# Kernel optimization log

Measured on AMD Instinct MI355X. Metric: run time of the kernel, lower is better.

## Reference

```python
import jax, jax.numpy as jnp
import numpy as np

NEG_SLOPE = 0.2


def gat_layer(x, src, dst, W, a_src, a_dst, b):
    # x: [N, Fin]; W: [Fin, H*C]; a_src/a_dst: [H, C]; b: [H*C]
    N = x.shape[0]
    H, C = a_src.shape
    h = (x @ W).reshape(N, H, C)                      # [N,H,C]
    s = jnp.einsum('nhc,hc->nh', h, a_src)            # alpha_src per node
    d = jnp.einsum('nhc,hc->nh', h, a_dst)            # alpha_dst per node
    e = jax.nn.leaky_relu(s[src] + d[dst], NEG_SLOPE) # [E,H]
    # segment softmax over incoming edges of each dst node
    m = jax.ops.segment_max(e, dst, num_segments=N)   # [N,H]
    ex = jnp.exp(e - m[dst])
    denom = jax.ops.segment_sum(ex, dst, num_segments=N)
    alpha = ex / (denom[dst] + 1e-16)                 # [E,H]
    out = jax.ops.segment_sum(h[src] * alpha[:, :, None], dst, num_segments=N)
    return out.reshape(N, H * C) + b                  # concat heads (H=1)


def setup_inputs() -> dict:
    key = jax.random.key(0)
    ks = jax.random.split(key, 16)
    N, E, Fin, Hid, Out, Hd = 100000, 1600000, 128, 64, 64, 1
    inp = {
        'x': jax.random.normal(ks[0], (N, Fin), dtype=jnp.float32),
        'edge_index': jax.random.randint(ks[1], (2, E), 0, N, dtype=jnp.int64),
    }
    def glorot(k, shape):
        fan = shape[0] + shape[-1]
        return jax.random.normal(k, shape, dtype=jnp.float32) * np.sqrt(2.0 / fan)
    inp['W1'] = glorot(ks[2], (Fin, Hd * Hid))
    inp['a1_src'] = glorot(ks[3], (Hd, Hid))
    inp['a1_dst'] = glorot(ks[4], (Hd, Hid))
    inp['b1'] = jnp.zeros((Hd * Hid,), dtype=jnp.float32)
    inp['W2'] = glorot(ks[5], (Hid, Hd * Hid))
    inp['a2_src'] = glorot(ks[6], (Hd, Hid))
    inp['a2_dst'] = glorot(ks[7], (Hd, Hid))
    inp['b2'] = jnp.zeros((Hd * Hid,), dtype=jnp.float32)
    inp['W3'] = glorot(ks[8], (Hid, Hd * Hid))
    inp['a3_src'] = glorot(ks[9], (Hd, Hid))
    inp['a3_dst'] = glorot(ks[10], (Hd, Hid))
    inp['b3'] = jnp.zeros((Hd * Hid,), dtype=jnp.float32)
    inp['fc_w'] = glorot(ks[11], (Hid, Out))
    inp['fc_b'] = jnp.zeros((Out,), dtype=jnp.float32)
    return inp


def reference(x, edge_index, W1, a1_src, a1_dst, b1, W2, a2_src, a2_dst, b2,
              W3, a3_src, a3_dst, b3, fc_w, fc_b):
    N = x.shape[0]
    loop = jnp.arange(N, dtype=edge_index.dtype)      # PyG add_self_loops
    src = jnp.concatenate([edge_index[0], loop])
    dst = jnp.concatenate([edge_index[1], loop])
    h = gat_layer(x, src, dst, W1, a1_src, a1_dst, b1)
    h = gat_layer(h, src, dst, W2, a2_src, a2_dst, b2)
    h = gat_layer(h, src, dst, W3, a3_src, a3_dst, b3)
    return h @ fc_w + fc_b
```

## Files before the change

### kernel.cpp

```cpp
#include <hip/hip_runtime.h>
#include <hip/hip_bf16.h>

typedef unsigned short u16;
typedef unsigned int u32;

__device__ __forceinline__ float wred_max(float v) {
    #pragma unroll
    for (int m = 32; m; m >>= 1) v = fmaxf(v, __shfl_xor(v, m, 64));
    return v;
}
__device__ __forceinline__ float wred_sum(float v) {
    #pragma unroll
    for (int m = 32; m; m >>= 1) v += __shfl_xor(v, m, 64);
    return v;
}
__device__ __forceinline__ u16 f2b(float f) {
    u32 u = __float_as_uint(f);
    u32 r = (u + 0x7FFFu + ((u >> 16) & 1u)) >> 16;
    return (u16)r;
}
__device__ __forceinline__ float blo(u32 u) { return __uint_as_float(u << 16); }
__device__ __forceinline__ float bhi(u32 u) { return __uint_as_float(u & 0xFFFF0000u); }

#define BIN_SHIFT 8
#define BIN_CHUNK 4096
#define MAXBINS 512

__global__ __launch_bounds__(256) void k_bin_gemm1(
    const int* __restrict__ ei, int E, int nbins, int binb, int cap,
    int* __restrict__ gcount, unsigned* __restrict__ rec,
    const float* __restrict__ in, const float* __restrict__ W,
    const float* __restrict__ asrc, const float* __restrict__ adst,
    u16* __restrict__ outh, float* __restrict__ sv, float* __restrict__ dv, int N)
{
    constexpr int K = 128;
    __shared__ float smem[64 * 64 + 64 * 64];
    const int tid = threadIdx.x;

    if (blockIdx.x < (unsigned)binb) {
        int* hist = (int*)smem;
        int* base = hist + MAXBINS;
        const int cbase = blockIdx.x * BIN_CHUNK;
        const int EN = E + N;

        for (int b = tid; b < nbins; b += 256) hist[b] = 0;
        __syncthreads();

        int srcs[16], dsts[16];
        #pragma unroll
        for (int i = 0; i < 16; i++) {
            int t = cbase + i * 256 + tid;
            int s = 0, d = -1;
            if (t < EN) {
                if (t < E) { s = ei[t]; d = ei[E + t]; }
                else       { s = t - E; d = s; }
                atomicAdd(&hist[d >> BIN_SHIFT], 1);
            }
            srcs[i] = s; dsts[i] = d;
        }
        __syncthreads();
        for (int b = tid; b < nbins; b += 256) {
            int h = hist[b];
            base[b] = h ? atomicAdd(&gcount[b], h) : 0;
        }
        __syncthreads();
        for (int b = tid; b < nbins; b += 256) hist[b] = 0;
        __syncthreads();
        #pragma unroll
        for (int i = 0; i < 16; i++) {
            int d = dsts[i];
            if (d >= 0) {
                int bin = d >> BIN_SHIFT;
                int r = atomicAdd(&hist[bin], 1);
                int idx = bin * cap + base[bin] + r;
                rec[idx] = (unsigned)srcs[i] | ((unsigned)(d & ((1 << BIN_SHIFT) - 1)) << 24);
            }
        }
        return;
    }

    float* Wl = smem;
    float* Xl = smem + 64 * 64;
    const int base = (blockIdx.x - binb) * 64;

    const int c4 = (tid & 15) << 2;
    const int r4 = (tid >> 4) << 2;

    float acc[4][4];
    #pragma unroll
    for (int i = 0; i < 4; i++)
        #pragma unroll
        for (int j = 0; j < 4; j++) acc[i][j] = 0.f;

    #define FMA4(i, XC, WV) \
        acc[i][0] += (XC) * (WV).x; acc[i][1] += (XC) * (WV).y; \
        acc[i][2] += (XC) * (WV).z; acc[i][3] += (XC) * (WV).w;

    for (int kt = 0; kt < K; kt += 64) {
        __syncthreads();
        for (int i = tid * 4; i < 64 * 64; i += 1024)
            *reinterpret_cast<float4*>(Wl + i) =
                *reinterpret_cast<const float4*>(W + (size_t)kt * 64 + i);
        for (int i = tid * 4; i < 64 * 64; i += 1024) {
            int node = i >> 6;
            int k = i & 63;
            float4 v = make_float4(0.f, 0.f, 0.f, 0.f);
            int gn = base + node;
            if (gn < N) v = *reinterpret_cast<const float4*>(in + (size_t)gn * K + kt + k);
            *reinterpret_cast<float4*>(Xl + node * 64 + (k ^ ((node & 7) << 2))) = v;
        }
        __syncthreads();

        for (int k0 = 0; k0 < 64; k0 += 4) {
            float4 wv0 = *reinterpret_cast<const float4*>(Wl + (k0 + 0) * 64 + c4);
            float4 wv1 = *reinterpret_cast<const float4*>(Wl + (k0 + 1) * 64 + c4);
            float4 wv2 = *reinterpret_cast<const float4*>(Wl + (k0 + 2) * 64 + c4);
            float4 wv3 = *reinterpret_cast<const float4*>(Wl + (k0 + 3) * 64 + c4);
            #pragma unroll
            for (int i = 0; i < 4; i++) {
                int node = r4 + i;
                float4 xv = *reinterpret_cast<const float4*>(
                    Xl + node * 64 + (k0 ^ ((node & 7) << 2)));
                FMA4(i, xv.x, wv0)
                FMA4(i, xv.y, wv1)
                FMA4(i, xv.z, wv2)
                FMA4(i, xv.w, wv3)
            }
        }
    }
    #undef FMA4

    const float4 as = *reinterpret_cast<const float4*>(asrc + c4);
    const float4 ad = *reinterpret_cast<const float4*>(adst + c4);
    #pragma unroll
    for (int i = 0; i < 4; i++) {
        int node = base + r4 + i;
        float ps = acc[i][0] * as.x + acc[i][1] * as.y
                 + acc[i][2] * as.z + acc[i][3] * as.w;
        float pd = acc[i][0] * ad.x + acc[i][1] * ad.y
                 + acc[i][2] * ad.z + acc[i][3] * ad.w;
        #pragma unroll
        for (int m = 1; m < 16; m <<= 1) {
            ps += __shfl_xor(ps, m, 64);
            pd += __shfl_xor(pd, m, 64);
        }
        if (node < N) {
            ushort4 o;
            o.x = f2b(acc[i][0]); o.y = f2b(acc[i][1]);
            o.z = f2b(acc[i][2]); o.w = f2b(acc[i][3]);
            *reinterpret_cast<ushort4*>(outh + ((size_t)node << 6) + c4) = o;
            if ((tid & 15) == 0) { sv[node] = ps; dv[node] = pd; }
        }
    }
}

__global__ __launch_bounds__(256) void k_unbin(
    const unsigned* __restrict__ rec, const int* __restrict__ gcount,
    int cap, int N, int* __restrict__ deg, int* __restrict__ colvp)
{
    __shared__ int cnt[1 << BIN_SHIFT];
    const int b = blockIdx.x;
    const int tid = threadIdx.x;
    const int node0 = b << BIN_SHIFT;
    cnt[tid] = 0;
    __syncthreads();
    int count = min(gcount[b], cap);
    for (int i = tid; i < count; i += 256) {
        unsigned r = rec[(size_t)b * cap + i];
        int s  = (int)(r & 0xFFFFFFu);
        int dl = (int)(r >> 24);
        int pos = atomicAdd(&cnt[dl], 1);
        if (pos < 64) colvp[((size_t)(node0 + dl) << 6) + pos] = s;
    }
    __syncthreads();
    int n = node0 + tid;
    if (n < N) deg[n] = min(cnt[tid], 64);
}

template<bool FUSE_SD>
__global__ __launch_bounds__(256) void k_gemm64(
    const float* __restrict__ in, const float* __restrict__ W,
    const float* __restrict__ asrc, const float* __restrict__ adst,
    const float* __restrict__ bias, void* __restrict__ out_,
    float* __restrict__ sv, float* __restrict__ dv, int N)
{
    constexpr int K = 64;
    __shared__ float Wl[K * 64];
    __shared__ float Xl[64 * K];
    const int tid  = threadIdx.x;
    const int base = blockIdx.x * 64;

    for (int i = tid * 4; i < K * 64; i += 1024)
        *reinterpret_cast<float4*>(Wl + i) = *reinterpret_cast<const float4*>(W + i);

    for (int i = tid * 4; i < 64 * K; i += 1024) {
        int node = i >> 6;
        int k = i & (K - 1);
        float4 v = make_float4(0.f, 0.f, 0.f, 0.f);
        int gn = base + node;
        if (gn < N) v = *reinterpret_cast<const float4*>(in + (size_t)gn * K + k);
        *reinterpret_cast<float4*>(Xl + node * K + (k ^ ((node & 7) << 2))) = v;
    }
    __syncthreads();

    const int c4 = (tid & 15) << 2;
    const int r4 = (tid >> 4) << 2;

    float acc[4][4];
    #pragma unroll
    for (int i = 0; i < 4; i++)
        #pragma unroll
        for (int j = 0; j < 4; j++) acc[i][j] = 0.f;

    #define FMA4(i, XC, WV) \
        acc[i][0] += (XC) * (WV).x; acc[i][1] += (XC) * (WV).y; \
        acc[i][2] += (XC) * (WV).z; acc[i][3] += (XC) * (WV).w;

    for (int k0 = 0; k0 < K; k0 += 4) {
        float4 wv0 = *reinterpret_cast<const float4*>(Wl + (k0 + 0) * 64 + c4);
        float4 wv1 = *reinterpret_cast<const float4*>(Wl + (k0 + 1) * 64 + c4);
        float4 wv2 = *reinterpret_cast<const float4*>(Wl + (k0 + 2) * 64 + c4);
        float4 wv3 = *reinterpret_cast<const float4*>(Wl + (k0 + 3) * 64 + c4);
        #pragma unroll
        for (int i = 0; i < 4; i++) {
            int node = r4 + i;
            float4 xv = *reinterpret_cast<const float4*>(
                Xl + node * K + (k0 ^ ((node & 7) << 2)));
            FMA4(i, xv.x, wv0)
            FMA4(i, xv.y, wv1)
            FMA4(i, xv.z, wv2)
            FMA4(i, xv.w, wv3)
        }
    }
    #undef FMA4

    if (FUSE_SD) {
        u16* outh = (u16*)out_;
        const float4 as = *reinterpret_cast<const float4*>(asrc + c4);
        const float4 ad = *reinterpret_cast<const float4*>(adst + c4);
        #pragma unroll
        for (int i = 0; i < 4; i++) {
            int node = base + r4 + i;
            float ps = acc[i][0] * as.x + acc[i][1] * as.y
                     + acc[i][2] * as.z + acc[i][3] * as.w;
            float pd = acc[i][0] * ad.x + acc[i][1] * ad.y
                     + acc[i][2] * ad.z + acc[i][3] * ad.w;
            #pragma unroll
            for (int m = 1; m < 16; m <<= 1) {
                ps += __shfl_xor(ps, m, 64);
                pd += __shfl_xor(pd, m, 64);
            }
            if (node < N) {
                ushort4 o;
                o.x = f2b(acc[i][0]); o.y = f2b(acc[i][1]);
                o.z = f2b(acc[i][2]); o.w = f2b(acc[i][3]);
                *reinterpret_cast<ushort4*>(outh + ((size_t)node << 6) + c4) = o;
                if ((tid & 15) == 0) { sv[node] = ps; dv[node] = pd; }
            }
        }
    } else {
        float* outf = (float*)out_;
        const float4 bv = *reinterpret_cast<const float4*>(bias + c4);
        #pragma unroll
        for (int i = 0; i < 4; i++) {
            int node = base + r4 + i;
            if (node < N) {
                *reinterpret_cast<float4*>(outf + ((size_t)node << 6) + c4) =
                    make_float4(acc[i][0] + bv.x, acc[i][1] + bv.y,
                                acc[i][2] + bv.z, acc[i][3] + bv.w);
            }
        }
    }
}

__global__ __launch_bounds__(256) void k_agg(
    const int* __restrict__ colv, const int* __restrict__ degarr,
    const float* __restrict__ sv, const float* __restrict__ dv,
    const u16* __restrict__ hb, const float* __restrict__ bias,
    float* __restrict__ out, int N)
{
    int n = blockIdx.x * 4 + (threadIdx.x >> 6);
    if (n >= N) return;
    int lane = threadIdx.x & 63;
    int r0 = n << 6;
    int deg = min(degarr[n], 64);
    float dn = dv[n];

    int sj = 0; float e = -3.4e38f;
    if (lane < deg) {
        sj = colv[r0 + lane];
        float t = sv[sj] + dn;
        e = t > 0.f ? t : 0.2f * t;
    }
    float m = wred_max(e);
    float p = (lane < deg) ? __expf(e - m) : 0.f;
    float den = wred_sum(p) + 1e-16f;
    p *= (1.0f / den);

    const int g  = lane >> 3;
    const int c8 = (lane & 7) << 3;
    const u16* hbase = hb + c8;
    const int dm1 = deg - 1;

    float acc[8];
    #pragma unroll
    for (int i = 0; i < 8; i++) acc[i] = 0.f;

    for (int j0 = 0; j0 < deg; j0 += 32) {
        int m0 = j0 + g;
        int m1 = m0 + 8, m2 = m0 + 16, m3 = m0 + 24;
        int cc0 = min(m0, dm1), cc1 = min(m1, dm1);
        int cc2 = min(m2, dm1), cc3 = min(m3, dm1);
        float a0 = __shfl(p, cc0, 64); int s0 = __shfl(sj, cc0, 64);
        float a1 = __shfl(p, cc1, 64); int s1 = __shfl(sj, cc1, 64);
        float a2 = __shfl(p, cc2, 64); int s2 = __shfl(sj, cc2, 64);
        float a3 = __shfl(p, cc3, 64); int s3 = __shfl(sj, cc3, 64);
        if (m1 > dm1) a1 = 0.f;
        if (m2 > dm1) a2 = 0.f;
        if (m3 > dm1) a3 = 0.f;
        uint4 u0 = make_uint4(0u,0u,0u,0u), u1 = u0, u2 = u0, u3 = u0;
        if (m0 <= dm1) u0 = *reinterpret_cast<const uint4*>(hbase + ((size_t)s0 << 6));
        if (m1 <= dm1) u1 = *reinterpret_cast<const uint4*>(hbase + ((size_t)s1 << 6));
        if (m2 <= dm1) u2 = *reinterpret_cast<const uint4*>(hbase + ((size_t)s2 << 6));
        if (m3 <= dm1) u3 = *reinterpret_cast<const uint4*>(hbase + ((size_t)s3 << 6));
        acc[0] += a0 * blo(u0.x); acc[1] += a0 * bhi(u0.x);
        acc[2] += a0 * blo(u0.y); acc[3] += a0 * bhi(u0.y);
        acc[4] += a0 * blo(u0.z); acc[5] += a0 * bhi(u0.z);
        acc[6] += a0 * blo(u0.w); acc[7] += a0 * bhi(u0.w);
        acc[0] += a1 * blo(u1.x); acc[1] += a1 * bhi(u1.x);
        acc[2] += a1 * blo(u1.y); acc[3] += a1 * bhi(u1.y);
        acc[4] += a1 * blo(u1.z); acc[5] += a1 * bhi(u1.z);
        acc[6] += a1 * blo(u1.w); acc[7] += a1 * bhi(u1.w);
        acc[0] += a2 * blo(u2.x); acc[1] += a2 * bhi(u2.x);
        acc[2] += a2 * blo(u2.y); acc[3] += a2 * bhi(u2.y);
        acc[4] += a2 * blo(u2.z); acc[5] += a2 * bhi(u2.z);
        acc[6] += a2 * blo(u2.w); acc[7] += a2 * bhi(u2.w);
        acc[0] += a3 * blo(u3.x); acc[1] += a3 * bhi(u3.x);
        acc[2] += a3 * blo(u3.y); acc[3] += a3 * bhi(u3.y);
        acc[4] += a3 * blo(u3.z); acc[5] += a3 * bhi(u3.z);
        acc[6] += a3 * blo(u3.w); acc[7] += a3 * bhi(u3.w);
    }
    #pragma unroll
    for (int mm = 8; mm <= 32; mm <<= 1) {
        #pragma unroll
        for (int i = 0; i < 8; i++) acc[i] += __shfl_xor(acc[i], mm, 64);
    }
    if (lane < 8) {
        const float4 b0 = *reinterpret_cast<const float4*>(bias + c8);
        const float4 b1 = *reinterpret_cast<const float4*>(bias + c8 + 4);
        *reinterpret_cast<float4*>(out + ((size_t)n << 6) + c8) =
            make_float4(acc[0] + b0.x, acc[1] + b0.y, acc[2] + b0.z, acc[3] + b0.w);
        *reinterpret_cast<float4*>(out + ((size_t)n << 6) + c8 + 4) =
            make_float4(acc[4] + b1.x, acc[5] + b1.y, acc[6] + b1.z, acc[7] + b1.w);
    }
}

extern "C" void kernel_launch(void* const* d_in, const int* in_sizes, int n_in,
                              void* d_out, int out_size, void* d_ws, size_t ws_size,
                              hipStream_t stream)
{
    const float* x   = (const float*)d_in[0];
    const int*   ei  = (const int*)d_in[1];
    const float* W1  = (const float*)d_in[2];
    const float* a1s = (const float*)d_in[3];
    const float* a1d = (const float*)d_in[4];
    const float* b1  = (const float*)d_in[5];
    const float* W2  = (const float*)d_in[6];
    const float* a2s = (const float*)d_in[7];
    const float* a2d = (const float*)d_in[8];
    const float* b2  = (const float*)d_in[9];
    const float* W3  = (const float*)d_in[10];
    const float* a3s = (const float*)d_in[11];
    const float* a3d = (const float*)d_in[12];
    const float* b3  = (const float*)d_in[13];
    const float* fw  = (const float*)d_in[14];
    const float* fb  = (const float*)d_in[15];

    const int Hid = in_sizes[3];
    const int Fin = in_sizes[2] / Hid;
    const int N   = in_sizes[0] / Fin;
    const int E   = in_sizes[1] / 2;
    const int EN  = E + N;
    (void)n_in; (void)out_size; (void)ws_size;

    char* p = (char*)d_ws;
    auto alloc = [&](size_t bytes) -> char* {
        char* r = p; p += (bytes + 255) & ~(size_t)255; return r;
    };
    float* sv = (float*)alloc((size_t)N * 4);
    float* dv = (float*)alloc((size_t)N * 4);
    u16*   h0 = (u16*)  alloc((size_t)N * 64 * 2);
    float* h1 = (float*)alloc((size_t)N * 64 * 4);
    int*   deg = (int*)  alloc((size_t)N * 4);
    int*   gcount = (int*)alloc((size_t)MAXBINS * 4);
    int*   colvp  = (int*)alloc((size_t)N * 64 * 4);

    const int nbins = (N + (1 << BIN_SHIFT) - 1) >> BIN_SHIFT;
    const int binb  = (EN + BIN_CHUNK - 1) / BIN_CHUNK;
    int cap = ((EN / nbins) * 2 + 127) & ~127;
    unsigned* rec = (unsigned*)h1;

    int gb = (N + 63) / 64;
    int ab = (N + 3) / 4;
    float* out = (float*)d_out;

    hipMemsetAsync(gcount, 0, (size_t)nbins * 4, stream);
    k_bin_gemm1<<<binb + gb, 256, 0, stream>>>(ei, E, nbins, binb, cap, gcount, rec,
                                               x, W1, a1s, a1d, h0, sv, dv, N);
    k_unbin<<<nbins, 256, 0, stream>>>(rec, gcount, cap, N, deg, colvp);
    k_agg<<<ab, 256, 0, stream>>>(colvp, deg, sv, dv, h0, b1, h1, N);
    k_gemm64<true ><<<gb, 256, 0, stream>>>(h1, W2, a2s, a2d, nullptr, h0, sv, dv, N);
    k_agg<<<ab, 256, 0, stream>>>(colvp, deg, sv, dv, h0, b2, h1, N);
    k_gemm64<true ><<<gb, 256, 0, stream>>>(h1, W3, a3s, a3d, nullptr, h0, sv, dv, N);
    k_agg<<<ab, 256, 0, stream>>>(colvp, deg, sv, dv, h0, b3, h1, N);
    k_gemm64<false><<<gb, 256, 0, stream>>>(h1, fw, nullptr, nullptr, fb, out, nullptr, nullptr, N);
}
```

Measured before the change: 288.1 us.

## Process two low-degree nodes per wave in GAT aggregation

Each wave now handles two destination nodes. When both have degree at most 32, the wave splits into two 32-lane halves, each doing its own softmax and gather for one node. Otherwise it falls back to handling the two nodes one after the other with a simpler loop. With an average degree of about 17, most nodes used fewer than half the lanes, so this targets wasted lanes and redundant per-node overhead. The trade-offs are more divergent control flow and a serial fallback path that has less memory-level parallelism.

New measurement: 244.8 us. 15.0% less time.

```diff
diff --git a/kernel.cpp b/kernel.cpp
--- a/kernel.cpp
+++ b/kernel.cpp
@@ -279,79 +279,130 @@
     const u16* __restrict__ hb, const float* __restrict__ bias,
     float* __restrict__ out, int N)
 {
-    int n = blockIdx.x * 4 + (threadIdx.x >> 6);
-    if (n >= N) return;
-    int lane = threadIdx.x & 63;
-    int r0 = n << 6;
-    int deg = min(degarr[n], 64);
-    float dn = dv[n];
-
-    int sj = 0; float e = -3.4e38f;
-    if (lane < deg) {
-        sj = colv[r0 + lane];
-        float t = sv[sj] + dn;
-        e = t > 0.f ? t : 0.2f * t;
-    }
-    float m = wred_max(e);
-    float p = (lane < deg) ? __expf(e - m) : 0.f;
-    float den = wred_sum(p) + 1e-16f;
-    p *= (1.0f / den);
-
-    const int g  = lane >> 3;
-    const int c8 = (lane & 7) << 3;
-    const u16* hbase = hb + c8;
-    const int dm1 = deg - 1;
-
-    float acc[8];
-    #pragma unroll
-    for (int i = 0; i < 8; i++) acc[i] = 0.f;
-
-    for (int j0 = 0; j0 < deg; j0 += 32) {
-        int m0 = j0 + g;
-        int m1 = m0 + 8, m2 = m0 + 16, m3 = m0 + 24;
-        int cc0 = min(m0, dm1), cc1 = min(m1, dm1);
-        int cc2 = min(m2, dm1), cc3 = min(m3, dm1);
-        float a0 = __shfl(p, cc0, 64); int s0 = __shfl(sj, cc0, 64);
-        float a1 = __shfl(p, cc1, 64); int s1 = __shfl(sj, cc1, 64);
-        float a2 = __shfl(p, cc2, 64); int s2 = __shfl(sj, cc2, 64);
-        float a3 = __shfl(p, cc3, 64); int s3 = __shfl(sj, cc3, 64);
-        if (m1 > dm1) a1 = 0.f;
-        if (m2 > dm1) a2 = 0.f;
-        if (m3 > dm1) a3 = 0.f;
-        uint4 u0 = make_uint4(0u,0u,0u,0u), u1 = u0, u2 = u0, u3 = u0;
-        if (m0 <= dm1) u0 = *reinterpret_cast<const uint4*>(hbase + ((size_t)s0 << 6));
-        if (m1 <= dm1) u1 = *reinterpret_cast<const uint4*>(hbase + ((size_t)s1 << 6));
-        if (m2 <= dm1) u2 = *reinterpret_cast<const uint4*>(hbase + ((size_t)s2 << 6));
-        if (m3 <= dm1) u3 = *reinterpret_cast<const uint4*>(hbase + ((size_t)s3 << 6));
-        acc[0] += a0 * blo(u0.x); acc[1] += a0 * bhi(u0.x);
-        acc[2] += a0 * blo(u0.y); acc[3] += a0 * bhi(u0.y);
-        acc[4] += a0 * blo(u0.z); acc[5] += a0 * bhi(u0.z);
-        acc[6] += a0 * blo(u0.w); acc[7] += a0 * bhi(u0.w);
-        acc[0] += a1 * blo(u1.x); acc[1] += a1 * bhi(u1.x);
-        acc[2] += a1 * blo(u1.y); acc[3] += a1 * bhi(u1.y);
-        acc[4] += a1 * blo(u1.z); acc[5] += a1 * bhi(u1.z);
-        acc[6] += a1 * blo(u1.w); acc[7] += a1 * bhi(u1.w);
-        acc[0] += a2 * blo(u2.x); acc[1] += a2 * bhi(u2.x);
-        acc[2] += a2 * blo(u2.y); acc[3] += a2 * bhi(u2.y);
-        acc[4] += a2 * blo(u2.z); acc[5] += a2 * bhi(u2.z);
-        acc[6] += a2 * blo(u2.w); acc[7] += a2 * bhi(u2.w);
-        acc[0] += a3 * blo(u3.x); acc[1] += a3 * bhi(u3.x);
-        acc[2] += a3 * blo(u3.y); acc[3] += a3 * bhi(u3.y);
-        acc[4] += a3 * blo(u3.z); acc[5] += a3 * bhi(u3.z);
-        acc[6] += a3 * blo(u3.w); acc[7] += a3 * bhi(u3.w);
-    }
-    #pragma unroll
-    for (int mm = 8; mm <= 32; mm <<= 1) {
-        #pragma unroll
-        for (int i = 0; i < 8; i++) acc[i] += __shfl_xor(acc[i], mm, 64);
-    }
-    if (lane < 8) {
-        const float4 b0 = *reinterpret_cast<const float4*>(bias + c8);
-        const float4 b1 = *reinterpret_cast<const float4*>(bias + c8 + 4);
-        *reinterpret_cast<float4*>(out + ((size_t)n << 6) + c8) =
-            make_float4(acc[0] + b0.x, acc[1] + b0.y, acc[2] + b0.z, acc[3] + b0.w);
-        *reinterpret_cast<float4*>(out + ((size_t)n << 6) + c8 + 4) =
-            make_float4(acc[4] + b1.x, acc[5] + b1.y, acc[6] + b1.z, acc[7] + b1.w);
+    const int lane = threadIdx.x & 63;
+    const int wave = threadIdx.x >> 6;
+    const int n0 = blockIdx.x * 8 + wave * 2;
+    if (n0 >= N) return;
+
+    int dA = min(degarr[n0], 64);
+    int dB = (n0 + 1 < N) ? min(degarr[n0 + 1], 64) : 0;
+
+    if (dA <= 32 && dB <= 32) {
+        const int half = lane >> 5;
+        const int l32  = lane & 31;
+        const int n    = n0 + half;
+        const bool nv  = (n < N);
+        const int deg  = half ? dB : dA;
+        const int r0   = n << 6;
+
+        int sj = 0; float e = -3.4e38f;
+        if (nv && l32 < deg) {
+            sj = colv[r0 + l32];
+            float t = sv[sj] + dv[n];
+            e = t > 0.f ? t : 0.2f * t;
+        }
+        float m = e;
+        #pragma unroll
+        for (int mm = 16; mm; mm >>= 1) m = fmaxf(m, __shfl_xor(m, mm, 64));
+        float p = (l32 < deg) ? __expf(e - m) : 0.f;
+        float s = p;
+        #pragma unroll
+        for (int mm = 16; mm; mm >>= 1) s += __shfl_xor(s, mm, 64);
+        p *= (1.0f / (s + 1e-16f));
+
+        const int g2 = l32 >> 3;
+        const int c8 = (l32 & 7) << 3;
+        const u16* hbase = hb + c8;
+        const int dm1 = deg - 1;
+        const int sb  = half << 5;
+
+        float acc[8];
+        #pragma unroll
+        for (int i = 0; i < 8; i++) acc[i] = 0.f;
+
+        for (int j0 = 0; j0 < deg; j0 += 8) {
+            int m0 = j0 + g2;
+            int m1 = m0 + 4;
+            int cc0 = min(m0, dm1), cc1 = min(m1, dm1);
+            float a0 = __shfl(p, sb + cc0, 64); int s0 = __shfl(sj, sb + cc0, 64);
+            float a1 = __shfl(p, sb + cc1, 64); int s1 = __shfl(sj, sb + cc1, 64);
+            if (m0 > dm1) a0 = 0.f;
+            if (m1 > dm1) a1 = 0.f;
+            uint4 u0 = make_uint4(0u,0u,0u,0u), u1 = u0;
+            if (m0 <= dm1) u0 = *reinterpret_cast<const uint4*>(hbase + ((size_t)s0 << 6));
+            if (m1 <= dm1) u1 = *reinterpret_cast<const uint4*>(hbase + ((size_t)s1 << 6));
+            acc[0] += a0 * blo(u0.x); acc[1] += a0 * bhi(u0.x);
+            acc[2] += a0 * blo(u0.y); acc[3] += a0 * bhi(u0.y);
+            acc[4] += a0 * blo(u0.z); acc[5] += a0 * bhi(u0.z);
+            acc[6] += a0 * blo(u0.w); acc[7] += a0 * bhi(u0.w);
+            acc[0] += a1 * blo(u1.x); acc[1] += a1 * bhi(u1.x);
+            acc[2] += a1 * blo(u1.y); acc[3] += a1 * bhi(u1.y);
+            acc[4] += a1 * blo(u1.z); acc[5] += a1 * bhi(u1.z);
+            acc[6] += a1 * blo(u1.w); acc[7] += a1 * bhi(u1.w);
+        }
+        #pragma unroll
+        for (int mm = 8; mm <= 16; mm <<= 1) {
+            #pragma unroll
+            for (int i = 0; i < 8; i++) acc[i] += __shfl_xor(acc[i], mm, 64);
+        }
+        if (nv && l32 < 8) {
+            const float4 b0 = *reinterpret_cast<const float4*>(bias + c8);
+            const float4 b1 = *reinterpret_cast<const float4*>(bias + c8 + 4);
+            *reinterpret_cast<float4*>(out + ((size_t)n << 6) + c8) =
+                make_float4(acc[0] + b0.x, acc[1] + b0.y, acc[2] + b0.z, acc[3] + b0.w);
+            *reinterpret_cast<float4*>(out + ((size_t)n << 6) + c8 + 4) =
+                make_float4(acc[4] + b1.x, acc[5] + b1.y, acc[6] + b1.z, acc[7] + b1.w);
+        }
+    } else {
+        for (int k = 0; k < 2; k++) {
+            int n = n0 + k;
+            if (n >= N) break;
+            int deg = min(degarr[n], 64);
+            int r0 = n << 6;
+            float dn = dv[n];
+            int sj = 0; float e = -3.4e38f;
+            if (lane < deg) {
+                sj = colv[r0 + lane];
+                float t = sv[sj] + dn;
+                e = t > 0.f ? t : 0.2f * t;
+            }
+            float m = wred_max(e);
+            float p = (lane < deg) ? __expf(e - m) : 0.f;
+            float den = wred_sum(p) + 1e-16f;
+            p *= (1.0f / den);
+
+            const int g  = lane >> 3;
+            const int c8 = (lane & 7) << 3;
+            const u16* hbase = hb + c8;
+            float acc[8];
+            #pragma unroll
+            for (int i = 0; i < 8; i++) acc[i] = 0.f;
+            for (int j = 0; j < deg; j += 8) {
+                int myj = j + g;
+                float a = __shfl(p,  myj & 63, 64);
+                int   s = __shfl(sj, myj & 63, 64);
+                if (myj < deg) {
+                    uint4 uv = *reinterpret_cast<const uint4*>(hbase + ((size_t)s << 6));
+                    acc[0] += a * blo(uv.x); acc[1] += a * bhi(uv.x);
+                    acc[2] += a * blo(uv.y); acc[3] += a * bhi(uv.y);
+                    acc[4] += a * blo(uv.z); acc[5] += a * bhi(uv.z);
+                    acc[6] += a * blo(uv.w); acc[7] += a * bhi(uv.w);
+                }
+            }
+            #pragma unroll
+            for (int mm = 8; mm <= 32; mm <<= 1) {
+                #pragma unroll
+                for (int i = 0; i < 8; i++) acc[i] += __shfl_xor(acc[i], mm, 64);
+            }
+            if (lane < 8) {
+                const float4 b0 = *reinterpret_cast<const float4*>(bias + c8);
+                const float4 b1 = *reinterpret_cast<const float4*>(bias + c8 + 4);
+                *reinterpret_cast<float4*>(out + ((size_t)n << 6) + c8) =
+                    make_float4(acc[0] + b0.x, acc[1] + b0.y, acc[2] + b0.z, acc[3] + b0.w);
+                *reinterpret_cast<float4*>(out + ((size_t)n << 6) + c8 + 4) =
+                    make_float4(acc[4] + b1.x, acc[5] + b1.y, acc[6] + b1.z, acc[7] + b1.w);
+            }
+        }
     }
 }
 
@@ -401,7 +452,7 @@
     unsigned* rec = (unsigned*)h1;
 
     int gb = (N + 63) / 64;
-    int ab = (N + 3) / 4;
+    int ab = (N + 7) / 8;
     float* out = (float*)d_out;
 
     hipMemsetAsync(gcount, 0, (size_t)nbins * 4, stream);
```
